# Performance work log

Hardware: AMD Instinct MI355X
Metric: run time of the kernel (lower is better)

The kernel has to match this reference:

```python
import jax, jax.numpy as jnp
import numpy as np

NUM_HEADS = 8
EMBED_CH = 512   # k channels
OUT_CH = 256     # v channels
MASK_CURRENT = False
NEG_INF = -1e30


def setup_inputs() -> dict:
    key = jax.random.key(0)
    ks = jax.random.split(key, 7)
    N, C, H, W = 8, 256, 32, 32
    s = lambda fan: 1.0 / np.sqrt(fan)
    return {
        "x": jax.random.normal(ks[0], (N, C, H, W), jnp.float32),
        "Wq": jax.random.normal(ks[1], (EMBED_CH, C), jnp.float32) * s(C),
        "bq": jax.random.normal(ks[2], (EMBED_CH,), jnp.float32) * 0.01,
        "Wkv": jax.random.normal(ks[3], (EMBED_CH + OUT_CH, C), jnp.float32) * s(C),
        "bkv": jax.random.normal(ks[4], (EMBED_CH + OUT_CH,), jnp.float32) * 0.01,
        "Wo": jax.random.normal(ks[5], (OUT_CH, OUT_CH), jnp.float32) * s(OUT_CH),
        "bo": jax.random.normal(ks[6], (OUT_CH,), jnp.float32) * 0.01,
    }


def _to_multihead(t, n, T):
    # t: [n, h*d, T] with channel layout '(h d)' -> [n, h, T, d]
    h = NUM_HEADS
    return t.reshape(n, h, -1, T).transpose(0, 1, 3, 2)


def reference(x, Wq, bq, Wkv, bkv, Wo, bo):
    n, C, H, W = x.shape
    T = H * W
    xf = x.reshape(n, C, T)  # flatten spatial dims into sequence

    # 1x1 convs == pointwise channel GEMMs
    q = jnp.einsum('oc,nct->not', Wq, xf) + bq[None, :, None]
    kv = jnp.einsum('oc,nct->not', Wkv, xf) + bkv[None, :, None]
    k, v = kv[:, :EMBED_CH], kv[:, EMBED_CH:]

    q = _to_multihead(q, n, T)   # [n, h, T, dk]
    k = _to_multihead(k, n, T)   # [n, h, T, dk]
    v = _to_multihead(v, n, T)   # [n, h, T, dv]

    dk = k.shape[-1]
    scale = 1.0 / np.sqrt(dk).astype(np.float32)

    # causal mask over flattened spatial positions (lower-triangular)
    diag = -1 if MASK_CURRENT else 0
    mask = jnp.tril(jnp.ones((T, T), dtype=bool), k=diag)  # [T, T]

    attn = jnp.einsum('nhtd,nhsd->nhts', q, k) * scale
    attn = jnp.where(mask[None, None], attn, NEG_INF)
    attn = jax.nn.softmax(attn, axis=-1)
    attn = jnp.where(mask[None, None], attn, 0.0)

    out = jnp.einsum('nhts,nhsd->nhtd', attn, v)            # [n, h, T, dv]
    out = out.transpose(0, 1, 3, 2).reshape(n, OUT_CH, T)   # n (h d) t

    out = jnp.einsum('oc,nct->not', Wo, out) + bo[None, :, None]
    return out.reshape(n, OUT_CH, H, W)
```

## Files before the change

kernel.cpp:

```cpp
#include <hip/hip_runtime.h>
#include <hip/hip_bf16.h>
#include <math.h>

typedef __bf16 bf16;
typedef __attribute__((ext_vector_type(4))) __bf16 bf16x4;
typedef __attribute__((ext_vector_type(8))) __bf16 bf16x8;
typedef __attribute__((ext_vector_type(4))) float f32x4;

#define T_DIM 1024
#define C_DIM 256
#define HEADS 8

static __device__ __forceinline__ int tb(int row, int col) {
  return row * 128 + ((((col >> 3) ^ row) & 7) << 4) + ((col & 7) << 1);
}

__global__ __launch_bounds__(256) void k_prep(const float* __restrict__ x,
    const float* __restrict__ Wq, const float* __restrict__ Wkv, const float* __restrict__ Wo,
    char* __restrict__ xTt, char* __restrict__ Wbt, char* __restrict__ Wot) {
  const int tid = threadIdx.x;
  const int b = blockIdx.x;
  if (b < 512) {
    __shared__ float tile[64][65];
    const int n = b >> 6, rem = b & 63, tt64 = rem >> 2, ct = (rem & 3) << 6;
    const float* xp = x + ((size_t)n * C_DIM + ct) * T_DIM + tt64 * 64;
    const int t4 = (tid & 15) * 4, c0 = tid >> 4;
#pragma unroll
    for (int i = 0; i < 4; ++i) {
      const int c = c0 + i * 16;
      float4 v = *(const float4*)(xp + (size_t)c * T_DIM + t4);
      tile[c][t4] = v.x; tile[c][t4 + 1] = v.y; tile[c][t4 + 2] = v.z; tile[c][t4 + 3] = v.w;
    }
    __syncthreads();
    char* dst = xTt + (((size_t)(n * 8 + (tt64 >> 1))) * 4 + (rem & 3)) * 16384;
    const int rbase = (tt64 & 1) * 64;
#pragma unroll
    for (int i = 0; i < 2; ++i) {
      const int idx = tid + i * 256;
      const int tl = idx >> 3, c8 = (idx & 7) * 8;
      bf16x8 v;
#pragma unroll
      for (int j = 0; j < 8; ++j) v[j] = (bf16)tile[c8 + j][tl];
      *(bf16x8*)(dst + tb(rbase + tl, c8)) = v;
    }
  } else {
    const bool isWo = (b >= 532);
    const int o0 = (b - (isWo ? 532 : 512)) * 64;
#pragma unroll
    for (int i = 0; i < 8; ++i) {
      const int idx = tid + i * 256;
      const int row = idx >> 5, c8 = (idx & 31) * 8;
      const int o = o0 + row;
      const float* src = isWo ? (Wo + (size_t)o * C_DIM + c8)
                              : (o < 512 ? Wq + (size_t)o * C_DIM + c8
                                         : Wkv + (size_t)(o - 512) * C_DIM + c8);
      float4 a = *(const float4*)src;
      float4 bq4 = *(const float4*)(src + 4);
      bf16x8 v;
      v[0]=(bf16)a.x; v[1]=(bf16)a.y; v[2]=(bf16)a.z; v[3]=(bf16)a.w;
      v[4]=(bf16)bq4.x; v[5]=(bf16)bq4.y; v[6]=(bf16)bq4.z; v[7]=(bf16)bq4.w;
      char* base = isWo ? Wot : Wbt;
      char* dst = base + (((size_t)(o >> 7)) * 4 + (c8 >> 6)) * 16384;
      *(bf16x8*)(dst + tb(o & 127, c8 & 63)) = v;
    }
  }
}

__global__ __launch_bounds__(256) void k_qkv(const char* __restrict__ Wbt, const char* __restrict__ xTt,
    const float* __restrict__ bq, const float* __restrict__ bkv,
    bf16* __restrict__ q_ws, char* __restrict__ Kt, char* __restrict__ Vt) {
  __shared__ __attribute__((aligned(128))) unsigned char smem[34816];
  const int tid = threadIdx.x;
  const int nt = blockIdx.x, mt = blockIdx.y, n = blockIdx.z;
  const int w = tid >> 6, lane = tid & 63, lrow = lane & 15, lg = lane >> 4;
  const int wm = (w >> 1) * 64, wn = (w & 1) * 64;
  const char* gA = Wbt + (size_t)mt * 65536;
  const char* gB = xTt + ((size_t)(n * 8 + nt)) * 65536;
  const float s2 = 0.18033688f;
  const int coff = w * 1024 + lane * 16;

  bf16x8 sA0, sA1, sA2, sA3, sB0, sB1, sB2, sB3;
  auto issue = [&](int kk) {
    const char* a = gA + kk * 16384 + coff;
    sA0 = *(const bf16x8*)(a);         sA1 = *(const bf16x8*)(a + 4096);
    sA2 = *(const bf16x8*)(a + 8192);  sA3 = *(const bf16x8*)(a + 12288);
    const char* bsrc = gB + kk * 16384 + coff;
    sB0 = *(const bf16x8*)(bsrc);        sB1 = *(const bf16x8*)(bsrc + 4096);
    sB2 = *(const bf16x8*)(bsrc + 8192); sB3 = *(const bf16x8*)(bsrc + 12288);
  };

  f32x4 acc[4][4] = {};
  issue(0);
#pragma unroll 1
  for (int kk = 0; kk < 4; ++kk) {
    __syncthreads();
    char* da = (char*)smem + coff;
    *(bf16x8*)(da)         = sA0; *(bf16x8*)(da + 4096)  = sA1;
    *(bf16x8*)(da + 8192)  = sA2; *(bf16x8*)(da + 12288) = sA3;
    char* db = (char*)smem + 16384 + coff;
    *(bf16x8*)(db)         = sB0; *(bf16x8*)(db + 4096)  = sB1;
    *(bf16x8*)(db + 8192)  = sB2; *(bf16x8*)(db + 12288) = sB3;
    if (kk < 3) issue(kk + 1);
    __syncthreads();
    const char* As = (const char*)smem;
    const char* Bs = As + 16384;
    bf16x8 af[4][2], bv[4][2];
#pragma unroll
    for (int mi = 0; mi < 4; ++mi)
#pragma unroll
      for (int kh = 0; kh < 2; ++kh)
        af[mi][kh] = *(const bf16x8*)(As + tb(wm + mi * 16 + lrow, kh * 32 + lg * 8));
#pragma unroll
    for (int ni = 0; ni < 4; ++ni)
#pragma unroll
      for (int kh = 0; kh < 2; ++kh)
        bv[ni][kh] = *(const bf16x8*)(Bs + tb(wn + ni * 16 + lrow, kh * 32 + lg * 8));
#pragma unroll
    for (int kh = 0; kh < 2; ++kh)
#pragma unroll
      for (int mi = 0; mi < 4; ++mi)
#pragma unroll
        for (int ni = 0; ni < 4; ++ni)
          acc[mi][ni] = __builtin_amdgcn_mfma_f32_16x16x32_bf16(af[mi][kh], bv[ni][kh], acc[mi][ni], 0, 0, 0);
  }
  __syncthreads();

  const int obase = mt * 128 + wm + lg * 4;
  const int tcol0 = nt * 128 + wn + lrow;
  if (mt < 8) {
#pragma unroll
    for (int mi = 0; mi < 4; ++mi) {
      const int o = obase + mi * 16;
      if (mt < 4) {
        const float4 bb = *(const float4*)(bq + o);
        const int nh = n * 8 + (o >> 6), d = o & 63;
        bf16* qrow = q_ws + (size_t)nh * (T_DIM * 64) + d;
#pragma unroll
        for (int ni = 0; ni < 4; ++ni) {
          const int t = tcol0 + ni * 16;
          f32x4 v = acc[mi][ni];
          bf16x4 pk;
          pk[0]=(bf16)((v[0]+bb.x)*s2); pk[1]=(bf16)((v[1]+bb.y)*s2);
          pk[2]=(bf16)((v[2]+bb.z)*s2); pk[3]=(bf16)((v[3]+bb.w)*s2);
          *(bf16x4*)(qrow + (size_t)t * 64) = pk;
        }
      } else {
        const int o2 = o - 512;
        const float4 bb = *(const float4*)(bkv + o2);
        const int nh = n * 8 + (o2 >> 6), d = o2 & 63;
        char* tbase = Kt + (size_t)nh * 16 * 8192;
#pragma unroll
        for (int ni = 0; ni < 4; ++ni) {
          const int t = tcol0 + ni * 16;
          f32x4 v = acc[mi][ni];
          bf16x4 pk;
          pk[0]=(bf16)(v[0]+bb.x); pk[1]=(bf16)(v[1]+bb.y); pk[2]=(bf16)(v[2]+bb.z); pk[3]=(bf16)(v[3]+bb.w);
          *(bf16x4*)(tbase + (t >> 6) * 8192 + tb(t & 63, d)) = pk;
        }
      }
    }
  } else {
    bf16* tp = (bf16*)smem;
#pragma unroll
    for (int mi = 0; mi < 4; ++mi) {
      const int o3g = (mt - 8) * 128 + wm + mi * 16 + lg * 4;
      const float4 bb = *(const float4*)(bkv + 512 + o3g);
      const float* bbp = (const float*)&bb;
      const int o3l = wm + mi * 16 + lg * 4;
#pragma unroll
      for (int ni = 0; ni < 4; ++ni) {
        const int tl = wn + ni * 16 + lrow;
        f32x4 v = acc[mi][ni];
#pragma unroll
        for (int r = 0; r < 4; ++r)
          tp[(o3l + r) * 132 + tl] = (bf16)(v[r] + bbp[r]);
      }
    }
    __syncthreads();
    const int row = tid >> 1, half = tid & 1;
    const int o3 = (mt - 8) * 128 + row;
    const int nh = n * 8 + (o3 >> 5), dv = o3 & 31;
    char* tile = Vt + (size_t)nh * 16 * 4096 + (nt * 2 + half) * 4096;
    const bf16* src = tp + row * 132 + half * 64;
#pragma unroll
    for (int g = 0; g < 8; ++g) {
      bf16x4 lo = *(const bf16x4*)(src + g * 8);
      bf16x4 hi = *(const bf16x4*)(src + g * 8 + 4);
      bf16x8 vv;
      vv[0]=lo[0]; vv[1]=lo[1]; vv[2]=lo[2]; vv[3]=lo[3];
      vv[4]=hi[0]; vv[5]=hi[1]; vv[6]=hi[2]; vv[7]=hi[3];
      *(bf16x8*)(tile + tb(dv, g * 8)) = vv;
    }
  }
}

__global__ __launch_bounds__(256) void k_attn(const bf16* __restrict__ q_ws,
    const char* __restrict__ Kt, const char* __restrict__ Vt, char* __restrict__ attTt) {
  __shared__ __attribute__((aligned(128))) unsigned char smem[32768];
  const int tid = threadIdx.x;
  const int nh = blockIdx.x, qp = blockIdx.y;
  const int w = tid >> 6, lane = tid & 63, lrow = lane & 15, lg = lane >> 4;
  const int tl = w * 16 + lrow;
  const char* Ktb = Kt + (size_t)nh * 16 * 8192;
  const char* Vtb = Vt + (size_t)nh * 16 * 4096;
  const int n = nh >> 3, h = nh & 7;
  const int koff = w * 1024 + lane * 16;
  const int voff = (tid >> 6) * 1024 + (tid & 63) * 16;

  const int qt0 = qp, qt1 = 15 - qp;
  const int tg0 = qt0 * 64 + tl, tg1 = qt1 * 64 + tl;
  const bf16* qb0 = q_ws + ((size_t)nh * T_DIM + tg0) * 64;
  const bf16* qb1 = q_ws + ((size_t)nh * T_DIM + tg1) * 64;
  const bf16x8 qA0 = *(const bf16x8*)(qb0 + lg * 8);
  const bf16x8 qA1 = *(const bf16x8*)(qb0 + 32 + lg * 8);
  const bf16x8 qB0 = *(const bf16x8*)(qb1 + lg * 8);
  const bf16x8 qB1 = *(const bf16x8*)(qb1 + 32 + lg * 8);

  float l0 = 0.f, l1 = 0.f;
  f32x4 o0a = {}, o0b = {}, o1a = {}, o1b = {};

  bf16x8 s0, s1, s2, s3, s4, s5;
  auto issue = [&](int st2, bool has1) {
    const char* k0 = Ktb + (size_t)st2 * 8192 + koff;
    s0 = *(const bf16x8*)(k0);
    s1 = *(const bf16x8*)(k0 + 4096);
    s4 = *(const bf16x8*)(Vtb + (size_t)st2 * 4096 + voff);
    if (has1) {
      const char* k1 = k0 + 8192;
      s2 = *(const bf16x8*)(k1);
      s3 = *(const bf16x8*)(k1 + 4096);
      s5 = *(const bf16x8*)(Vtb + (size_t)(st2 + 1) * 4096 + voff);
    }
  };

  auto proc = [&](bf16x8 qf0, bf16x8 qf1, float& l, f32x4& oa, f32x4& ob,
                  const char* Kbs, const char* Vbs, char* pws, bool diag) {
    f32x4 sacc[4];
    __builtin_amdgcn_s_setprio(1);
#pragma unroll
    for (int rt = 0; rt < 4; ++rt) {
      f32x4 a = {0.f, 0.f, 0.f, 0.f};
      bf16x8 kf0 = *(const bf16x8*)(Kbs + tb(rt * 16 + lrow, lg * 8));
      a = __builtin_amdgcn_mfma_f32_16x16x32_bf16(kf0, qf0, a, 0, 0, 0);
      bf16x8 kf1 = *(const bf16x8*)(Kbs + tb(rt * 16 + lrow, 32 + lg * 8));
      a = __builtin_amdgcn_mfma_f32_16x16x32_bf16(kf1, qf1, a, 0, 0, 0);
      sacc[rt] = a;
    }
    __builtin_amdgcn_s_setprio(0);
    float p[16];
#pragma unroll
    for (int rt = 0; rt < 4; ++rt)
#pragma unroll
      for (int r = 0; r < 4; ++r) {
        float e = __builtin_amdgcn_exp2f(sacc[rt][r]);
        if (diag && (rt * 16 + lg * 4 + r) > tl) e = 0.f;
        p[rt * 4 + r] = e;
      }
    float t0 = (p[0] + p[1]) + (p[2] + p[3]);
    float t1 = (p[4] + p[5]) + (p[6] + p[7]);
    float t2 = (p[8] + p[9]) + (p[10] + p[11]);
    float t3 = (p[12] + p[13]) + (p[14] + p[15]);
    float ps = (t0 + t1) + (t2 + t3);
    ps += __shfl_xor(ps, 16);
    ps += __shfl_xor(ps, 32);
    l += ps;
#pragma unroll
    for (int rt = 0; rt < 4; ++rt) {
      bf16x4 pk;
#pragma unroll
      for (int r = 0; r < 4; ++r) pk[r] = (bf16)p[rt * 4 + r];
      *(bf16x4*)(pws + tb(lrow, rt * 16 + lg * 4)) = pk;
    }
    __builtin_amdgcn_s_setprio(1);
#pragma unroll
    for (int ks = 0; ks < 2; ++ks) {
      bf16x8 pf = *(const bf16x8*)(pws + tb(lrow, ks * 32 + lg * 8));
      bf16x8 vf0 = *(const bf16x8*)(Vbs + tb(lrow, ks * 32 + lg * 8));
      oa = __builtin_amdgcn_mfma_f32_16x16x32_bf16(vf0, pf, oa, 0, 0, 0);
      bf16x8 vf1 = *(const bf16x8*)(Vbs + tb(16 + lrow, ks * 32 + lg * 8));
      ob = __builtin_amdgcn_mfma_f32_16x16x32_bf16(vf1, pf, ob, 0, 0, 0);
    }
    __builtin_amdgcn_s_setprio(0);
  };

  issue(0, 1 <= qt1);
#pragma unroll 1
  for (int st2 = 0; st2 <= qt1; st2 += 2) {
    const bool has1 = (st2 + 1 <= qt1);
    __syncthreads();
    {
      char* kd = (char*)smem + koff;
      *(bf16x8*)(kd) = s0;
      *(bf16x8*)(kd + 4096) = s1;
      *(bf16x8*)((char*)smem + 16384 + voff) = s4;
      if (has1) {
        *(bf16x8*)(kd + 8192) = s2;
        *(bf16x8*)(kd + 12288) = s3;
        *(bf16x8*)((char*)smem + 20480 + voff) = s5;
      }
    }
    const int nst2 = st2 + 2;
    if (nst2 <= qt1) issue(nst2, nst2 + 1 <= qt1);
    __syncthreads();
    const int nsub = has1 ? 2 : 1;
#pragma unroll 1
    for (int sub = 0; sub < nsub; ++sub) {
      const int stk = st2 + sub;
      const char* Kbs = (const char*)smem + sub * 8192;
      const char* Vbs = (const char*)smem + 16384 + sub * 4096;
      char* pws = (char*)smem + 24576 + w * 2048;
      proc(qB0, qB1, l1, o1a, o1b, Kbs, Vbs, pws, stk == qt1);
      if (stk <= qt0)
        proc(qA0, qA1, l0, o0a, o0b, Kbs, Vbs, pws, stk == qt0);
    }
  }

  auto epi = [&](int tg, float l, f32x4 oa, f32x4 ob) {
    const float inv = 1.0f / l;
    const int ntt = tg >> 7, row = tg & 127;
#pragma unroll
    for (int dt = 0; dt < 2; ++dt) {
      const f32x4 v = dt ? ob : oa;
      const int c = h * 32 + dt * 16 + lg * 4;
      char* tile = attTt + (((size_t)(n * 8 + ntt)) * 4 + (c >> 6)) * 16384;
      bf16x4 pk;
#pragma unroll
      for (int r = 0; r < 4; ++r) pk[r] = (bf16)(v[r] * inv);
      *(bf16x4*)(tile + tb(row, c & 63)) = pk;
    }
  };
  epi(tg0, l0, o0a, o0b);
  epi(tg1, l1, o1a, o1b);
}

__global__ __launch_bounds__(256) void k_proj(const char* __restrict__ attTt,
    const char* __restrict__ Wot, const float* __restrict__ bo, float* __restrict__ out) {
  __shared__ __attribute__((aligned(128))) unsigned char smem[16384];
  const int tid = threadIdx.x;
  const int tm = blockIdx.x, om = blockIdx.y, n = blockIdx.z;
  const int w = tid >> 6, lane = tid & 63, lrow = lane & 15, lg = lane >> 4;
  const int wm = (w >> 1) * 32, wn = (w & 1) * 32;
  const char* gA = attTt + ((size_t)(n * 8 + (tm >> 1))) * 65536 + (tm & 1) * 8192;
  const char* gB = Wot + (size_t)(om >> 1) * 65536 + (om & 1) * 8192;
  const int coff = w * 1024 + lane * 16;

  bf16x8 pA0, pA1, pB0, pB1;
  auto issue = [&](int kk) {
    const char* a = gA + kk * 16384 + coff;
    pA0 = *(const bf16x8*)(a); pA1 = *(const bf16x8*)(a + 4096);
    const char* bsrc = gB + kk * 16384 + coff;
    pB0 = *(const bf16x8*)(bsrc); pB1 = *(const bf16x8*)(bsrc + 4096);
  };

  f32x4 acc[2][2] = {};
  issue(0);
#pragma unroll 1
  for (int kk = 0; kk < 4; ++kk) {
    __syncthreads();
    char* da = (char*)smem + coff;
    *(bf16x8*)(da) = pA0; *(bf16x8*)(da + 4096) = pA1;
    char* db = (char*)smem + 8192 + coff;
    *(bf16x8*)(db) = pB0; *(bf16x8*)(db + 4096) = pB1;
    if (kk < 3) issue(kk + 1);
    __syncthreads();
    const char* As = (const char*)smem;
    const char* Bs = As + 8192;
    bf16x8 af[2][2], bv[2][2];
#pragma unroll
    for (int mi = 0; mi < 2; ++mi)
#pragma unroll
      for (int kh = 0; kh < 2; ++kh)
        af[mi][kh] = *(const bf16x8*)(As + tb(wm + mi * 16 + lrow, kh * 32 + lg * 8));
#pragma unroll
    for (int ni = 0; ni < 2; ++ni)
#pragma unroll
      for (int kh = 0; kh < 2; ++kh)
        bv[ni][kh] = *(const bf16x8*)(Bs + tb(wn + ni * 16 + lrow, kh * 32 + lg * 8));
#pragma unroll
    for (int kh = 0; kh < 2; ++kh)
#pragma unroll
      for (int mi = 0; mi < 2; ++mi)
#pragma unroll
        for (int ni = 0; ni < 2; ++ni)
          acc[mi][ni] = __builtin_amdgcn_mfma_f32_16x16x32_bf16(af[mi][kh], bv[ni][kh], acc[mi][ni], 0, 0, 0);
  }

  const int t0b = tm * 64 + wm + lg * 4;
  const int ob = om * 64 + wn + lrow;
#pragma unroll
  for (int mi = 0; mi < 2; ++mi) {
    const int t0 = t0b + mi * 16;
#pragma unroll
    for (int ni = 0; ni < 2; ++ni) {
      const int o = ob + ni * 16;
      const float bb = bo[o];
      f32x4 v = acc[mi][ni];
      v[0] += bb; v[1] += bb; v[2] += bb; v[3] += bb;
      *(f32x4*)(out + ((size_t)(n * C_DIM + o)) * T_DIM + t0) = v;
    }
  }
}

extern "C" void kernel_launch(void* const* d_in, const int* in_sizes, int n_in,
                              void* d_out, int out_size, void* d_ws, size_t ws_size,
                              hipStream_t stream) {
  const float* x   = (const float*)d_in[0];
  const float* Wq  = (const float*)d_in[1];
  const float* bq  = (const float*)d_in[2];
  const float* Wkv = (const float*)d_in[3];
  const float* bkv = (const float*)d_in[4];
  const float* Wo  = (const float*)d_in[5];
  const float* bo  = (const float*)d_in[6];
  float* out = (float*)d_out;

  char* ws = (char*)d_ws;
  char* xTt   = ws;
  char* Wbt   = ws + (4u  << 20);
  char* Wot   = ws + (5u  << 20);
  bf16* q_ws  = (bf16*)(ws + (6u << 20));
  char* Kt    = ws + (14u << 20);
  char* Vt    = ws + (22u << 20);
  char* attTt = ws + (26u << 20);

  k_prep<<<536, 256, 0, stream>>>(x, Wq, Wkv, Wo, xTt, Wbt, Wot);
  k_qkv<<<dim3(8, 10, 8), 256, 0, stream>>>(Wbt, xTt, bq, bkv, q_ws, Kt, Vt);
  k_attn<<<dim3(64, 8), 256, 0, stream>>>(q_ws, Kt, Vt, attTt);
  k_proj<<<dim3(16, 4, 8), 256, 0, stream>>>(attTt, Wot, bo, out);
}
```

Baseline: 50.19 us.

## Split attention into one query tile per block and halve projection tile rows

```diff
diff --git a/kernel.cpp b/kernel.cpp
--- a/kernel.cpp
+++ b/kernel.cpp
@@ -198,109 +198,53 @@
     const char* __restrict__ Kt, const char* __restrict__ Vt, char* __restrict__ attTt) {
   __shared__ __attribute__((aligned(128))) unsigned char smem[32768];
   const int tid = threadIdx.x;
-  const int nh = blockIdx.x, qp = blockIdx.y;
+  const int nh = blockIdx.x, qt = blockIdx.y;
   const int w = tid >> 6, lane = tid & 63, lrow = lane & 15, lg = lane >> 4;
   const int tl = w * 16 + lrow;
   const char* Ktb = Kt + (size_t)nh * 16 * 8192;
   const char* Vtb = Vt + (size_t)nh * 16 * 4096;
   const int n = nh >> 3, h = nh & 7;
-  const int koff = w * 1024 + lane * 16;
-  const int voff = (tid >> 6) * 1024 + (tid & 63) * 16;
-
-  const int qt0 = qp, qt1 = 15 - qp;
-  const int tg0 = qt0 * 64 + tl, tg1 = qt1 * 64 + tl;
-  const bf16* qb0 = q_ws + ((size_t)nh * T_DIM + tg0) * 64;
-  const bf16* qb1 = q_ws + ((size_t)nh * T_DIM + tg1) * 64;
-  const bf16x8 qA0 = *(const bf16x8*)(qb0 + lg * 8);
-  const bf16x8 qA1 = *(const bf16x8*)(qb0 + 32 + lg * 8);
-  const bf16x8 qB0 = *(const bf16x8*)(qb1 + lg * 8);
-  const bf16x8 qB1 = *(const bf16x8*)(qb1 + 32 + lg * 8);
-
-  float l0 = 0.f, l1 = 0.f;
-  f32x4 o0a = {}, o0b = {}, o1a = {}, o1b = {};
+  const int coff = tid * 16;
+
+  const int tg = qt * 64 + tl;
+  const bf16* qb = q_ws + ((size_t)nh * T_DIM + tg) * 64;
+  const bf16x8 qf0 = *(const bf16x8*)(qb + lg * 8);
+  const bf16x8 qf1 = *(const bf16x8*)(qb + 32 + lg * 8);
+
+  float l = 0.f;
+  f32x4 oa = {}, ob = {};
 
   bf16x8 s0, s1, s2, s3, s4, s5;
   auto issue = [&](int st2, bool has1) {
-    const char* k0 = Ktb + (size_t)st2 * 8192 + koff;
+    const char* k0 = Ktb + (size_t)st2 * 8192 + coff;
     s0 = *(const bf16x8*)(k0);
     s1 = *(const bf16x8*)(k0 + 4096);
-    s4 = *(const bf16x8*)(Vtb + (size_t)st2 * 4096 + voff);
+    s4 = *(const bf16x8*)(Vtb + (size_t)st2 * 4096 + coff);
     if (has1) {
-      const char* k1 = k0 + 8192;
-      s2 = *(const bf16x8*)(k1);
-      s3 = *(const bf16x8*)(k1 + 4096);
-      s5 = *(const bf16x8*)(Vtb + (size_t)(st2 + 1) * 4096 + voff);
+      s2 = *(const bf16x8*)(k0 + 8192);
+      s3 = *(const bf16x8*)(k0 + 12288);
+      s5 = *(const bf16x8*)(Vtb + (size_t)(st2 + 1) * 4096 + coff);
     }
   };
 
-  auto proc = [&](bf16x8 qf0, bf16x8 qf1, float& l, f32x4& oa, f32x4& ob,
-                  const char* Kbs, const char* Vbs, char* pws, bool diag) {
-    f32x4 sacc[4];
-    __builtin_amdgcn_s_setprio(1);
-#pragma unroll
-    for (int rt = 0; rt < 4; ++rt) {
-      f32x4 a = {0.f, 0.f, 0.f, 0.f};
-      bf16x8 kf0 = *(const bf16x8*)(Kbs + tb(rt * 16 + lrow, lg * 8));
-      a = __builtin_amdgcn_mfma_f32_16x16x32_bf16(kf0, qf0, a, 0, 0, 0);
-      bf16x8 kf1 = *(const bf16x8*)(Kbs + tb(rt * 16 + lrow, 32 + lg * 8));
-      a = __builtin_amdgcn_mfma_f32_16x16x32_bf16(kf1, qf1, a, 0, 0, 0);
-      sacc[rt] = a;
-    }
-    __builtin_amdgcn_s_setprio(0);
-    float p[16];
-#pragma unroll
-    for (int rt = 0; rt < 4; ++rt)
-#pragma unroll
-      for (int r = 0; r < 4; ++r) {
-        float e = __builtin_amdgcn_exp2f(sacc[rt][r]);
-        if (diag && (rt * 16 + lg * 4 + r) > tl) e = 0.f;
-        p[rt * 4 + r] = e;
-      }
-    float t0 = (p[0] + p[1]) + (p[2] + p[3]);
-    float t1 = (p[4] + p[5]) + (p[6] + p[7]);
-    float t2 = (p[8] + p[9]) + (p[10] + p[11]);
-    float t3 = (p[12] + p[13]) + (p[14] + p[15]);
-    float ps = (t0 + t1) + (t2 + t3);
-    ps += __shfl_xor(ps, 16);
-    ps += __shfl_xor(ps, 32);
-    l += ps;
-#pragma unroll
-    for (int rt = 0; rt < 4; ++rt) {
-      bf16x4 pk;
-#pragma unroll
-      for (int r = 0; r < 4; ++r) pk[r] = (bf16)p[rt * 4 + r];
-      *(bf16x4*)(pws + tb(lrow, rt * 16 + lg * 4)) = pk;
-    }
-    __builtin_amdgcn_s_setprio(1);
-#pragma unroll
-    for (int ks = 0; ks < 2; ++ks) {
-      bf16x8 pf = *(const bf16x8*)(pws + tb(lrow, ks * 32 + lg * 8));
-      bf16x8 vf0 = *(const bf16x8*)(Vbs + tb(lrow, ks * 32 + lg * 8));
-      oa = __builtin_amdgcn_mfma_f32_16x16x32_bf16(vf0, pf, oa, 0, 0, 0);
-      bf16x8 vf1 = *(const bf16x8*)(Vbs + tb(16 + lrow, ks * 32 + lg * 8));
-      ob = __builtin_amdgcn_mfma_f32_16x16x32_bf16(vf1, pf, ob, 0, 0, 0);
-    }
-    __builtin_amdgcn_s_setprio(0);
-  };
-
-  issue(0, 1 <= qt1);
+  issue(0, 1 <= qt);
 #pragma unroll 1
-  for (int st2 = 0; st2 <= qt1; st2 += 2) {
-    const bool has1 = (st2 + 1 <= qt1);
+  for (int st2 = 0; st2 <= qt; st2 += 2) {
+    const bool has1 = (st2 + 1 <= qt);
     __syncthreads();
     {
-      char* kd = (char*)smem + koff;
+      char* kd = (char*)smem + coff;
       *(bf16x8*)(kd) = s0;
       *(bf16x8*)(kd + 4096) = s1;
-      *(bf16x8*)((char*)smem + 16384 + voff) = s4;
+      *(bf16x8*)((char*)smem + 16384 + coff) = s4;
       if (has1) {
         *(bf16x8*)(kd + 8192) = s2;
         *(bf16x8*)(kd + 12288) = s3;
-        *(bf16x8*)((char*)smem + 20480 + voff) = s5;
+        *(bf16x8*)((char*)smem + 20480 + coff) = s5;
       }
     }
     const int nst2 = st2 + 2;
-    if (nst2 <= qt1) issue(nst2, nst2 + 1 <= qt1);
+    if (nst2 <= qt) issue(nst2, nst2 + 1 <= qt);
     __syncthreads();
     const int nsub = has1 ? 2 : 1;
 #pragma unroll 1
@@ -309,68 +253,105 @@
       const char* Kbs = (const char*)smem + sub * 8192;
       const char* Vbs = (const char*)smem + 16384 + sub * 4096;
       char* pws = (char*)smem + 24576 + w * 2048;
-      proc(qB0, qB1, l1, o1a, o1b, Kbs, Vbs, pws, stk == qt1);
-      if (stk <= qt0)
-        proc(qA0, qA1, l0, o0a, o0b, Kbs, Vbs, pws, stk == qt0);
-    }
-  }
-
-  auto epi = [&](int tg, float l, f32x4 oa, f32x4 ob) {
-    const float inv = 1.0f / l;
-    const int ntt = tg >> 7, row = tg & 127;
-#pragma unroll
-    for (int dt = 0; dt < 2; ++dt) {
-      const f32x4 v = dt ? ob : oa;
-      const int c = h * 32 + dt * 16 + lg * 4;
-      char* tile = attTt + (((size_t)(n * 8 + ntt)) * 4 + (c >> 6)) * 16384;
-      bf16x4 pk;
-#pragma unroll
-      for (int r = 0; r < 4; ++r) pk[r] = (bf16)(v[r] * inv);
-      *(bf16x4*)(tile + tb(row, c & 63)) = pk;
-    }
-  };
-  epi(tg0, l0, o0a, o0b);
-  epi(tg1, l1, o1a, o1b);
+      const bool diag = (stk == qt);
+
+      f32x4 sacc[4];
+      __builtin_amdgcn_s_setprio(1);
+#pragma unroll
+      for (int rt = 0; rt < 4; ++rt) {
+        f32x4 a = {0.f, 0.f, 0.f, 0.f};
+        bf16x8 kf0 = *(const bf16x8*)(Kbs + tb(rt * 16 + lrow, lg * 8));
+        a = __builtin_amdgcn_mfma_f32_16x16x32_bf16(kf0, qf0, a, 0, 0, 0);
+        bf16x8 kf1 = *(const bf16x8*)(Kbs + tb(rt * 16 + lrow, 32 + lg * 8));
+        a = __builtin_amdgcn_mfma_f32_16x16x32_bf16(kf1, qf1, a, 0, 0, 0);
+        sacc[rt] = a;
+      }
+      __builtin_amdgcn_s_setprio(0);
+      float p[16];
+#pragma unroll
+      for (int rt = 0; rt < 4; ++rt)
+#pragma unroll
+        for (int r = 0; r < 4; ++r) {
+          float e = __builtin_amdgcn_exp2f(sacc[rt][r]);
+          if (diag && (rt * 16 + lg * 4 + r) > tl) e = 0.f;
+          p[rt * 4 + r] = e;
+        }
+      float t0 = (p[0] + p[1]) + (p[2] + p[3]);
+      float t1 = (p[4] + p[5]) + (p[6] + p[7]);
+      float t2 = (p[8] + p[9]) + (p[10] + p[11]);
+      float t3 = (p[12] + p[13]) + (p[14] + p[15]);
+      float ps = (t0 + t1) + (t2 + t3);
+      ps += __shfl_xor(ps, 16);
+      ps += __shfl_xor(ps, 32);
+      l += ps;
+#pragma unroll
+      for (int rt = 0; rt < 4; ++rt) {
+        bf16x4 pk;
+#pragma unroll
+        for (int r = 0; r < 4; ++r) pk[r] = (bf16)p[rt * 4 + r];
+        *(bf16x4*)(pws + tb(lrow, rt * 16 + lg * 4)) = pk;
+      }
+      __builtin_amdgcn_s_setprio(1);
+#pragma unroll
+      for (int ks = 0; ks < 2; ++ks) {
+        bf16x8 pf = *(const bf16x8*)(pws + tb(lrow, ks * 32 + lg * 8));
+        bf16x8 vf0 = *(const bf16x8*)(Vbs + tb(lrow, ks * 32 + lg * 8));
+        oa = __builtin_amdgcn_mfma_f32_16x16x32_bf16(vf0, pf, oa, 0, 0, 0);
+        bf16x8 vf1 = *(const bf16x8*)(Vbs + tb(16 + lrow, ks * 32 + lg * 8));
+        ob = __builtin_amdgcn_mfma_f32_16x16x32_bf16(vf1, pf, ob, 0, 0, 0);
+      }
+      __builtin_amdgcn_s_setprio(0);
+    }
+  }
+
+  const float inv = 1.0f / l;
+  const int ntt = tg >> 7, row = tg & 127;
+#pragma unroll
+  for (int dt = 0; dt < 2; ++dt) {
+    const f32x4 v = dt ? ob : oa;
+    const int c = h * 32 + dt * 16 + lg * 4;
+    char* tile = attTt + (((size_t)(n * 8 + ntt)) * 4 + (c >> 6)) * 16384;
+    bf16x4 pk;
+#pragma unroll
+    for (int r = 0; r < 4; ++r) pk[r] = (bf16)(v[r] * inv);
+    *(bf16x4*)(tile + tb(row, c & 63)) = pk;
+  }
 }
 
 __global__ __launch_bounds__(256) void k_proj(const char* __restrict__ attTt,
     const char* __restrict__ Wot, const float* __restrict__ bo, float* __restrict__ out) {
-  __shared__ __attribute__((aligned(128))) unsigned char smem[16384];
+  __shared__ __attribute__((aligned(128))) unsigned char smem[12288];
   const int tid = threadIdx.x;
   const int tm = blockIdx.x, om = blockIdx.y, n = blockIdx.z;
   const int w = tid >> 6, lane = tid & 63, lrow = lane & 15, lg = lane >> 4;
-  const int wm = (w >> 1) * 32, wn = (w & 1) * 32;
-  const char* gA = attTt + ((size_t)(n * 8 + (tm >> 1))) * 65536 + (tm & 1) * 8192;
+  const int wm = (w >> 1) * 16, wn = (w & 1) * 32;
+  const char* gA = attTt + ((size_t)(n * 8 + (tm >> 2))) * 65536 + (tm & 3) * 4096;
   const char* gB = Wot + (size_t)(om >> 1) * 65536 + (om & 1) * 8192;
-  const int coff = w * 1024 + lane * 16;
-
-  bf16x8 pA0, pA1, pB0, pB1;
+  const int coff = tid * 16;
+
+  bf16x8 pA0, pB0, pB1;
   auto issue = [&](int kk) {
-    const char* a = gA + kk * 16384 + coff;
-    pA0 = *(const bf16x8*)(a); pA1 = *(const bf16x8*)(a + 4096);
+    pA0 = *(const bf16x8*)(gA + kk * 16384 + coff);
     const char* bsrc = gB + kk * 16384 + coff;
     pB0 = *(const bf16x8*)(bsrc); pB1 = *(const bf16x8*)(bsrc + 4096);
   };
 
-  f32x4 acc[2][2] = {};
+  f32x4 acc[2] = {};
   issue(0);
 #pragma unroll 1
   for (int kk = 0; kk < 4; ++kk) {
     __syncthreads();
-    char* da = (char*)smem + coff;
-    *(bf16x8*)(da) = pA0; *(bf16x8*)(da + 4096) = pA1;
-    char* db = (char*)smem + 8192 + coff;
+    if (coff < 4096) *(bf16x8*)((char*)smem + coff) = pA0;
+    char* db = (char*)smem + 4096 + coff;
     *(bf16x8*)(db) = pB0; *(bf16x8*)(db + 4096) = pB1;
     if (kk < 3) issue(kk + 1);
     __syncthreads();
     const char* As = (const char*)smem;
-    const char* Bs = As + 8192;
-    bf16x8 af[2][2], bv[2][2];
-#pragma unroll
-    for (int mi = 0; mi < 2; ++mi)
-#pragma unroll
-      for (int kh = 0; kh < 2; ++kh)
-        af[mi][kh] = *(const bf16x8*)(As + tb(wm + mi * 16 + lrow, kh * 32 + lg * 8));
+    const char* Bs = As + 4096;
+    bf16x8 af[2], bv[2][2];
+#pragma unroll
+    for (int kh = 0; kh < 2; ++kh)
+      af[kh] = *(const bf16x8*)(As + tb(wm + lrow, kh * 32 + lg * 8));
 #pragma unroll
     for (int ni = 0; ni < 2; ++ni)
 #pragma unroll
@@ -379,25 +360,18 @@
 #pragma unroll
     for (int kh = 0; kh < 2; ++kh)
 #pragma unroll
-      for (int mi = 0; mi < 2; ++mi)
-#pragma unroll
-        for (int ni = 0; ni < 2; ++ni)
-          acc[mi][ni] = __builtin_amdgcn_mfma_f32_16x16x32_bf16(af[mi][kh], bv[ni][kh], acc[mi][ni], 0, 0, 0);
-  }
-
-  const int t0b = tm * 64 + wm + lg * 4;
-  const int ob = om * 64 + wn + lrow;
-#pragma unroll
-  for (int mi = 0; mi < 2; ++mi) {
-    const int t0 = t0b + mi * 16;
-#pragma unroll
-    for (int ni = 0; ni < 2; ++ni) {
-      const int o = ob + ni * 16;
-      const float bb = bo[o];
-      f32x4 v = acc[mi][ni];
-      v[0] += bb; v[1] += bb; v[2] += bb; v[3] += bb;
-      *(f32x4*)(out + ((size_t)(n * C_DIM + o)) * T_DIM + t0) = v;
-    }
+      for (int ni = 0; ni < 2; ++ni)
+        acc[ni] = __builtin_amdgcn_mfma_f32_16x16x32_bf16(af[kh], bv[ni][kh], acc[ni], 0, 0, 0);
+  }
+
+  const int t0 = tm * 32 + wm + lg * 4;
+#pragma unroll
+  for (int ni = 0; ni < 2; ++ni) {
+    const int o = om * 64 + wn + ni * 16 + lrow;
+    const float bb = bo[o];
+    f32x4 v = acc[ni];
+    v[0] += bb; v[1] += bb; v[2] += bb; v[3] += bb;
+    *(f32x4*)(out + ((size_t)(n * C_DIM + o)) * T_DIM + t0) = v;
   }
 }
 
@@ -424,6 +398,6 @@
 
   k_prep<<<536, 256, 0, stream>>>(x, Wq, Wkv, Wo, xTt, Wbt, Wot);
   k_qkv<<<dim3(8, 10, 8), 256, 0, stream>>>(Wbt, xTt, bq, bkv, q_ws, Kt, Vt);
-  k_attn<<<dim3(64, 8), 256, 0, stream>>>(q_ws, Kt, Vt, attTt);
-  k_proj<<<dim3(16, 4, 8), 256, 0, stream>>>(attTt, Wot, bo, out);
-}
+  k_attn<<<dim3(64, 16), 256, 0, stream>>>(q_ws, Kt, Vt, attTt);
+  k_proj<<<dim3(32, 4, 8), 256, 0, stream>>>(attTt, Wot, bo, out);
+}
```

New measurement: 52.44 us. +4.5%, slower.
